# Kernel tuning notes

Hardware: AMD Instinct MI355X
Metric: run time of the kernel (lower is better)

The kernel has to match this reference:

```python
import jax, jax.numpy as jnp
import numpy as np

BLOCK, HALO, HEADS = 8, 4, 4


def setup_inputs() -> dict:
    key = jax.random.key(0)
    ks = jax.random.split(key, 9)
    B, C, H, W = 8, 256, 64, 64
    inner = C  # heads * dim_head = 4 * 64
    d = inner // HEADS
    R = BLOCK + 2 * HALO  # 16
    s = 0.02
    return {
        "x": jax.random.normal(ks[0], (B, C, H, W), jnp.float32),
        "wq": jax.random.normal(ks[1], (inner, C), jnp.float32) * s,
        "wkv": jax.random.normal(ks[2], (2 * inner, C), jnp.float32) * s,
        "wo": jax.random.normal(ks[3], (C, inner), jnp.float32) * s,
        "bo": jax.random.normal(ks[4], (C,), jnp.float32) * s,
        "rel_h": jax.random.normal(ks[5], (2 * R - 1, d), jnp.float32) * (d ** -0.5),
        "rel_w": jax.random.normal(ks[6], (2 * R - 1, d), jnp.float32) * (d ** -0.5),
        "w_conv": jax.random.normal(ks[7], (4 * C, C), jnp.float32) * s,
        "b_conv": jax.random.normal(ks[8], (4 * C,), jnp.float32) * s,
    }


def reference(x, wq, wkv, wo, bo, rel_h, rel_w, w_conv, b_conv):
    B, C, H, W = x.shape
    bs, halo, heads = BLOCK, HALO, HEADS
    R = bs + 2 * halo
    inner = wq.shape[0]
    d = inner // heads
    nh, nw = H // bs, W // bs
    Nb = B * nh * nw

    # ---- HaloAttention ----
    # block queries: (B, C, nh, bs, nw, bs) -> (Nb, bs*bs, C)
    q_in = x.reshape(B, C, nh, bs, nw, bs).transpose(0, 2, 4, 3, 5, 1).reshape(Nb, bs * bs, C)
    # haloed K/V windows via overlapping gather (== F.unfold(kernel=R, stride=bs, pad=halo))
    xp = jnp.pad(x, ((0, 0), (0, 0), (halo, halo), (halo, halo)))
    ridx = (jnp.arange(nh) * bs)[:, None] + jnp.arange(R)[None]  # (nh, R)
    cidx = (jnp.arange(nw) * bs)[:, None] + jnp.arange(R)[None]  # (nw, R)
    win = xp[:, :, ridx][:, :, :, :, cidx]                       # (B, C, nh, R, nw, R)
    kv_in = win.transpose(0, 2, 4, 3, 5, 1).reshape(Nb, R * R, C)

    q = (q_in @ wq.T).reshape(Nb, bs * bs, heads, d).transpose(0, 2, 1, 3) * (d ** -0.5)
    kv = kv_in @ wkv.T
    k, v = jnp.split(kv, 2, axis=-1)
    k = k.reshape(Nb, R * R, heads, d).transpose(0, 2, 1, 3)
    v = v.reshape(Nb, R * R, heads, d).transpose(0, 2, 1, 3)

    sim = jnp.einsum('bhid,bhjd->bhij', q, k)  # (Nb, heads, bs*bs, R*R)

    # relative position logits (computed from the scaled q, as in the torch code)
    q5 = q.reshape(Nb, heads, bs, bs, d)
    rel_idx = jnp.arange(R)[None, :] - jnp.arange(bs)[:, None] + (R - 1)  # (bs, R)
    lw = jnp.einsum('bhxyd,yjd->bhxyj', q5, rel_w[rel_idx])  # over key col j
    lh = jnp.einsum('bhxyd,xid->bhxyi', q5, rel_h[rel_idx])  # over key row i
    sim = sim.reshape(Nb, heads, bs, bs, R, R) + lw[..., None, :] + lh[..., None]
    sim = sim.reshape(Nb, heads, bs * bs, R * R)

    # mask out padded halo positions
    m = jnp.pad(jnp.ones((H, W), bool), ((halo, halo), (halo, halo)))
    mwin = m[ridx][:, :, cidx].transpose(0, 2, 1, 3).reshape(nh * nw, R * R)
    mask = jnp.broadcast_to(mwin[None], (B, nh * nw, R * R)).reshape(Nb, 1, 1, R * R)
    sim = jnp.where(mask, sim, -jnp.finfo(sim.dtype).max)

    attn = jax.nn.softmax(sim, axis=-1)
    out = jnp.einsum('bhij,bhjd->bhid', attn, v)
    out = out.transpose(0, 2, 1, 3).reshape(Nb, bs * bs, inner)
    out = out @ wo.T + bo  # (Nb, bs*bs, C)
    y = out.reshape(B, nh, nw, bs, bs, C).transpose(0, 5, 1, 3, 2, 4).reshape(B, C, H, W)

    # ---- Conv2d(dim, 4*dim, 1) + PixelShuffle(2) ----
    y = jnp.einsum('bchw,oc->bohw', y, w_conv) + b_conv[None, :, None, None]
    Cn = y.shape[1] // 4
    y = y.reshape(B, Cn, 2, 2, H, W).transpose(0, 1, 4, 2, 5, 3).reshape(B, Cn, 2 * H, 2 * W)
    return y
```

## Files before the change

### kernel.cpp

```cpp
#include <hip/hip_runtime.h>

typedef unsigned short u16;
typedef unsigned int u32;
typedef __attribute__((ext_vector_type(8))) short short8;
typedef __attribute__((ext_vector_type(4))) float f32x4;

__device__ __forceinline__ float bf2f(u16 u){ union { u32 i; float f; } x; x.i = ((u32)u)<<16; return x.f; }
__device__ __forceinline__ u16 f2bf(float f){ union { float f; u32 i; } x; x.f = f; u32 r = x.i + 0x7fffu + ((x.i>>16)&1u); return (u16)(r>>16); }

#define MFMA16(a,b,c) __builtin_amdgcn_mfma_f32_16x16x32_bf16((a),(b),(c),0,0,0)

__device__ __forceinline__ uint4 ld8(const void* p, size_t off, int f32) {
  if (f32) {
    const float* fp = (const float*)p + off;
    float4 a = *(const float4*)fp;
    float4 b = *(const float4*)(fp + 4);
    uint4 o;
    o.x = (u32)f2bf(a.x) | ((u32)f2bf(a.y)<<16);
    o.y = (u32)f2bf(a.z) | ((u32)f2bf(a.w)<<16);
    o.z = (u32)f2bf(b.x) | ((u32)f2bf(b.y)<<16);
    o.w = (u32)f2bf(b.z) | ((u32)f2bf(b.w)<<16);
    return o;
  }
  return *(const uint4*)((const u16*)p + off);
}
__device__ __forceinline__ uint2 ld4(const void* p, size_t off, int f32) {
  if (f32) {
    const float* fp = (const float*)p + off;
    float4 a = *(const float4*)fp;
    uint2 o;
    o.x = (u32)f2bf(a.x) | ((u32)f2bf(a.y)<<16);
    o.y = (u32)f2bf(a.z) | ((u32)f2bf(a.w)<<16);
    return o;
  }
  return *(const uint2*)((const u16*)p + off);
}
__device__ __forceinline__ float ldsc(const void* p, size_t off, int f32) {
  if (f32) return ((const float*)p)[off];
  return bf2f(((const u16*)p)[off]);
}

__global__ __launch_bounds__(256) void k_detect(const u32* __restrict__ x, int* __restrict__ flag)
{
  __shared__ int cnt;
  if (threadIdx.x == 0) cnt = 0;
  __syncthreads();
  int c = 0;
  #pragma unroll
  for (int i = 0; i < 32; ++i) {
    u32 w = x[threadIdx.x*32 + i];
    u32 e = (w >> 7) & 0xFFu;
    c += (e == 0u || (e >= 96u && e <= 143u)) ? 1 : 0;
  }
  atomicAdd(&cnt, c);
  __syncthreads();
  if (threadIdx.x == 0) *flag = (cnt < 4915) ? 1 : 0;
}

__global__ __launch_bounds__(256) void k_transpose(const void* __restrict__ x, u16* __restrict__ xt,
                                                   const int* __restrict__ flagp)
{
  __shared__ int sflag;
  __shared__ __align__(16) u16 tile[64][68];
  if (threadIdx.x == 0) sflag = *flagp;
  __syncthreads();
  const int f32 = sflag;
  const int p0 = blockIdx.x*64, c0 = blockIdx.y*64, b = blockIdx.z;
  const int t = threadIdx.x;
  const size_t xbo = ((size_t)(b*256 + c0))*4096 + p0;
  #pragma unroll
  for (int pass=0; pass<4; ++pass) {
    int cl = pass*16 + (t>>4);
    int pl = (t&15)*4;
    uint2 v = ld4(x, xbo + (size_t)cl*4096 + pl, f32);
    *(uint2*)&tile[cl][pl] = v;
  }
  __syncthreads();
  u16* xtb = xt + ((size_t)b*4096 + p0)*256 + c0;
  #pragma unroll
  for (int pass=0; pass<4; ++pass) {
    int pl = pass*16 + (t>>4);
    int cl = (t&15)*4;
    unsigned int lo = (unsigned int)tile[cl][pl]   | ((unsigned int)tile[cl+1][pl]<<16);
    unsigned int hi = (unsigned int)tile[cl+2][pl] | ((unsigned int)tile[cl+3][pl]<<16);
    uint2 o; o.x = lo; o.y = hi;
    *(uint2*)(xtb + (size_t)pl*256 + cl) = o;
  }
}

__global__ __launch_bounds__(256) void k_gemm_bt(
  const u16* __restrict__ A, const void* __restrict__ Bt, const void* __restrict__ bias,
  void* __restrict__ C, int M, int N, int K, float scale, int shuffle,
  const int* __restrict__ flagp)
{
  __shared__ int sflag;
  __shared__ __align__(16) char smem[20608];
  u16* Als = (u16*)smem;
  u16* Bls = (u16*)(smem + 10240);
  if (threadIdx.x == 0) sflag = *flagp;
  __syncthreads();
  const int f32 = sflag;
  const int m0 = blockIdx.x*128, n0 = blockIdx.y*128;
  const int t = threadIdx.x, lane = t & 63, wv = t >> 6;
  const int wm = (wv & 1)*64, wn = (wv >> 1)*64;
  const int lm = lane & 15, lq = lane >> 4;
  f32x4 acc[4][4] = {};
  for (int k0 = 0; k0 < K; k0 += 32) {
    #pragma unroll
    for (int i = 0; i < 2; ++i) {
      int u = t + i*256;
      int row = u >> 2, ch = (u & 3)*8;
      *(uint4*)&Als[row*40 + ch] = *(const uint4*)(A + (size_t)(m0+row)*K + k0 + ch);
      *(uint4*)&Bls[row*40 + ch] = ld8(Bt, (size_t)(n0+row)*K + k0 + ch, f32);
    }
    __syncthreads();
    short8 af[4], bf[4];
    #pragma unroll
    for (int i=0;i<4;++i) af[i] = *(const short8*)&Als[(wm + i*16 + lm)*40 + lq*8];
    #pragma unroll
    for (int i=0;i<4;++i) bf[i] = *(const short8*)&Bls[(wn + i*16 + lm)*40 + lq*8];
    #pragma unroll
    for (int mt=0;mt<4;++mt)
      #pragma unroll
      for (int nt=0;nt<4;++nt)
        acc[mt][nt] = MFMA16(af[mt], bf[nt], acc[mt][nt]);
    __syncthreads();
  }

  if (!shuffle) {
    u16* eh = (u16*)smem;
    #pragma unroll
    for (int c=0;c<2;++c) {
      __syncthreads();
      if ((wv>>1) == c) {
        #pragma unroll
        for (int nt=0;nt<4;++nt) {
          int col = n0 + c*64 + nt*16 + lm;
          float bv = bias ? ldsc(bias, col, f32) : 0.0f;
          #pragma unroll
          for (int mt=0;mt<4;++mt)
            #pragma unroll
            for (int r=0;r<4;++r) {
              int row = wm + mt*16 + lq*4 + r;
              eh[row*72 + nt*16 + lm] = f2bf(acc[mt][nt][r]*scale + bv);
            }
        }
      }
      __syncthreads();
      {
        int row = t >> 1, off = (t & 1)*32;
        const uint4* s = (const uint4*)&eh[row*72 + off];
        uint4 v0 = s[0], v1 = s[1], v2 = s[2], v3 = s[3];
        uint4* dp = (uint4*)((u16*)C + (size_t)(m0+row)*N + n0 + c*64 + off);
        dp[0]=v0; dp[1]=v1; dp[2]=v2; dp[3]=v3;
      }
    }
  } else {
    float* ef = (float*)smem;
    const int b = m0 >> 12;
    const int hh0 = (m0 & 4095) >> 6;
    #pragma unroll
    for (int c=0;c<4;++c) {
      __syncthreads();
      if ((wv>>1) == (c>>1)) {
        #pragma unroll
        for (int nt2=0;nt2<2;++nt2) {
          int nt = (c&1)*2 + nt2;
          int col = n0 + wn + nt*16 + lm;
          float bv = bias ? ldsc(bias, col, f32) : 0.0f;
          int col_rel = nt2*16 + lm;
          int cn_rel = col_rel >> 2, rr = (col_rel >> 1) & 1, ss = col_rel & 1;
          #pragma unroll
          for (int mt=0;mt<4;++mt)
            #pragma unroll
            for (int r=0;r<4;++r) {
              int row = wm + mt*16 + lq*4 + r;
              int orow = cn_rel*4 + (row>>6)*2 + rr;
              int ow   = (row & 63)*2 + ss;
              ef[orow*136 + ow] = acc[mt][nt][r]*scale + bv;
            }
        }
      }
      __syncthreads();
      {
        int orow = t >> 3, seg = t & 7;
        int cn_rel = orow >> 2, oh_rel = orow & 3;
        int cn = ((n0 + c*32) >> 2) + cn_rel;
        size_t obase = (((size_t)(b*256 + cn))*128 + hh0*2 + oh_rel)*128 + seg*16;
        const float4* s = (const float4*)&ef[orow*136 + seg*16];
        float4 v0 = s[0], v1 = s[1], v2 = s[2], v3 = s[3];
        if (f32) {
          float4* dp = (float4*)((float*)C + obase);
          dp[0]=v0; dp[1]=v1; dp[2]=v2; dp[3]=v3;
        } else {
          float vv[16];
          *(float4*)&vv[0]=v0; *(float4*)&vv[4]=v1; *(float4*)&vv[8]=v2; *(float4*)&vv[12]=v3;
          u32 pw[8];
          #pragma unroll
          for (int j=0;j<8;++j) pw[j] = (u32)f2bf(vv[2*j]) | ((u32)f2bf(vv[2*j+1])<<16);
          u16* dp = (u16*)C + obase;
          *(uint4*)dp       = *(uint4*)&pw[0];
          *(uint4*)(dp + 8) = *(uint4*)&pw[4];
        }
      }
    }
  }
}

#define MASKVAL (-30000.0f)
__global__ __launch_bounds__(256) void k_halo_attn(
  const u16* __restrict__ qo, const u16* __restrict__ kv,
  const void* __restrict__ relh, const void* __restrict__ relw,
  u16* __restrict__ aout, const int* __restrict__ flagp)
{
  __shared__ int sflag;
  __shared__ __align__(16) u16 Qs[64*72];
  __shared__ __align__(16) u16 KP[128*72];
  __shared__ __align__(16) u16 Vt[64*136];
  __shared__ __align__(16) u16 Gw[64*32];
  __shared__ __align__(16) u16 Gh[64*32];
  if (threadIdx.x == 0) sflag = *flagp;
  __syncthreads();
  const int f32 = sflag;

  const int blk = blockIdx.x, head = blockIdx.y;
  const int bb = blk >> 6, by = (blk >> 3) & 7, bx = blk & 7;
  const int h0 = by*8, w0 = bx*8;
  const int t = threadIdx.x, lane = t & 63, wv = t >> 6;
  const int lm = lane & 15, lq = lane >> 4;
  const size_t pixbase = (size_t)bb * 4096;
  const float LOG2E = 1.4426950408889634f;

  #pragma unroll
  for (int i=0;i<2;++i) {
    int u = t + i*256;
    int row = u >> 3, ch = (u & 7)*8;
    int qx = row >> 3, qy = row & 7;
    size_t p = pixbase + (size_t)(h0+qx)*64 + (w0+qy);
    *(uint4*)&Qs[row*72 + ch] = *(const uint4*)(qo + p*256 + head*64 + ch);
  }
  {
    u16* RW = KP; u16* RH = KP + 2048;
    if (t < 248) {
      *(uint4*)&RW[t*8] = ld8(relw, (size_t)t*8, f32);
      *(uint4*)&RH[t*8] = ld8(relh, (size_t)t*8, f32);
    } else {
      uint4 z; z.x=z.y=z.z=z.w=0;
      int o = 1984 + (t-248)*8;
      *(uint4*)&RW[o] = z;
      *(uint4*)&RH[o] = z;
    }
  }
  __syncthreads();
  {
    const u16* RW = KP; const u16* RH = KP + 2048;
    f32x4 agw[2] = {}, agh[2] = {};
    #pragma unroll
    for (int ks=0;ks<2;++ks) {
      short8 aq = *(const short8*)&Qs[(wv*16 + lm)*72 + ks*32 + lq*8];
      #pragma unroll
      for (int nt=0;nt<2;++nt) {
        short8 bw = *(const short8*)&RW[(nt*16 + lm)*64 + ks*32 + lq*8];
        short8 bh = *(const short8*)&RH[(nt*16 + lm)*64 + ks*32 + lq*8];
        agw[nt] = MFMA16(aq, bw, agw[nt]);
        agh[nt] = MFMA16(aq, bh, agh[nt]);
      }
    }
    #pragma unroll
    for (int nt=0;nt<2;++nt)
      #pragma unroll
      for (int r=0;r<4;++r) {
        int m = wv*16 + lq*4 + r, c = nt*16 + lm;
        Gw[m*32 + c] = f2bf(agw[nt][r]);
        Gh[m*32 + c] = f2bf(agh[nt][r]);
      }
  }
  __syncthreads();

  float m_run[4], l_run[4];
  #pragma unroll
  for (int r=0;r<4;++r){ m_run[r] = MASKVAL; l_run[r] = 0.0f; }
  f32x4 acc_o[4] = {};

  for (int tile=0; tile<2; ++tile) {
    #pragma unroll
    for (int i=0;i<4;++i) {
      int u = t + i*256;
      int kl = u >> 3, ch = (u & 7)*8;
      int ki = tile*8 + (kl >> 4), kj = kl & 15;
      int hk = h0 - 4 + ki, wk = w0 - 4 + kj;
      uint4 v; v.x=v.y=v.z=v.w=0;
      if ((unsigned)hk < 64u && (unsigned)wk < 64u) {
        size_t p = pixbase + (size_t)hk*64 + wk;
        v = *(const uint4*)(kv + p*512 + head*64 + ch);
      }
      *(uint4*)&KP[kl*72 + ch] = v;
    }
    {
      int kl = t & 127, db = (t >> 7)*32;
      int ki = tile*8 + (kl >> 4), kj = kl & 15;
      int hk = h0 - 4 + ki, wk = w0 - 4 + kj;
      bool ok = ((unsigned)hk < 64u) && ((unsigned)wk < 64u);
      size_t p = pixbase + (size_t)hk*64 + wk;
      const u16* vp = kv + p*512 + 256 + head*64 + db;
      #pragma unroll
      for (int c=0;c<4;++c) {
        union { uint4 v; u16 s[8]; } uu;
        uu.v.x=uu.v.y=uu.v.z=uu.v.w=0;
        if (ok) uu.v = *(const uint4*)(vp + c*8);
        #pragma unroll
        for (int jj=0;jj<8;++jj) Vt[(db + c*8 + jj)*136 + kl] = uu.s[jj];
      }
    }
    __syncthreads();
    f32x4 as[8] = {};
    #pragma unroll
    for (int ks=0;ks<2;++ks) {
      short8 aq = *(const short8*)&Qs[(wv*16 + lm)*72 + ks*32 + lq*8];
      #pragma unroll
      for (int nt=0;nt<8;++nt) {
        short8 bk = *(const short8*)&KP[(nt*16 + lm)*72 + ks*32 + lq*8];
        as[nt] = MFMA16(aq, bk, as[nt]);
      }
    }
    __syncthreads();
    #pragma unroll
    for (int r=0;r<4;++r) {
      int m = wv*16 + lq*4 + r;
      int qx = m >> 3, qy = m & 7;
      float vals[8]; float rowmax = MASKVAL;
      #pragma unroll
      for (int nt=0;nt<8;++nt) {
        int ki = tile*8 + nt;
        int hk = h0 - 4 + ki, wk = w0 - 4 + lm;
        float v = as[nt][r]
                + bf2f(Gw[m*32 + (lm - qy + 15)])
                + bf2f(Gh[m*32 + (ki - qx + 15)]);
        if (!((unsigned)hk < 64u && (unsigned)wk < 64u)) v = MASKVAL;
        vals[nt] = v;
        rowmax = fmaxf(rowmax, v);
      }
      #pragma unroll
      for (int s=1;s<16;s<<=1) rowmax = fmaxf(rowmax, __shfl_xor(rowmax, s, 64));
      float mnew = fmaxf(m_run[r], rowmax);
      float alpha = exp2f((m_run[r] - mnew)*LOG2E);
      float rs = 0.0f;
      #pragma unroll
      for (int nt=0;nt<8;++nt) {
        float e = exp2f((vals[nt] - mnew)*LOG2E);
        rs += e;
        KP[m*136 + nt*16 + lm] = f2bf(e);
      }
      #pragma unroll
      for (int s=1;s<16;s<<=1) rs += __shfl_xor(rs, s, 64);
      l_run[r] = l_run[r]*alpha + rs;
      m_run[r] = mnew;
      #pragma unroll
      for (int nt=0;nt<4;++nt) acc_o[nt][r] *= alpha;
    }
    __syncthreads();
    #pragma unroll
    for (int ks=0;ks<4;++ks) {
      short8 ap = *(const short8*)&KP[(wv*16 + lm)*136 + ks*32 + lq*8];
      #pragma unroll
      for (int nt=0;nt<4;++nt) {
        short8 bv = *(const short8*)&Vt[(nt*16 + lm)*136 + ks*32 + lq*8];
        acc_o[nt] = MFMA16(ap, bv, acc_o[nt]);
      }
    }
    __syncthreads();
  }
  #pragma unroll
  for (int nt=0;nt<4;++nt)
    #pragma unroll
    for (int r=0;r<4;++r) {
      int m = wv*16 + lq*4 + r;
      int qx = m >> 3, qy = m & 7;
      size_t p = pixbase + (size_t)(h0+qx)*64 + (w0+qy);
      aout[p*256 + head*64 + nt*16 + lm] = f2bf(acc_o[nt][r]/l_run[r]);
    }
}

extern "C" void kernel_launch(void* const* d_in, const int* in_sizes, int n_in,
                              void* d_out, int out_size, void* d_ws, size_t ws_size,
                              hipStream_t stream)
{
  const void* x     = d_in[0];
  const void* wq    = d_in[1];
  const void* wkv   = d_in[2];
  const void* wo    = d_in[3];
  const void* bo    = d_in[4];
  const void* relh  = d_in[5];
  const void* relw  = d_in[6];
  const void* wconv = d_in[7];
  const void* bconv = d_in[8];

  int* flag = (int*)d_ws;
  u16* y2   = (u16*)((char*)d_ws + 4096);
  u16* base = (u16*)d_out;
  u16* kvb  = base;
  u16* qo   = base + 16777216;
  u16* xt   = base + 25165824;
  u16* aout = qo;

  k_detect<<<1, 256, 0, stream>>>((const u32*)x, flag);
  k_transpose<<<dim3(64,4,8), 256, 0, stream>>>(x, xt, flag);
  k_gemm_bt<<<dim3(256,2), 256, 0, stream>>>(xt, wq,  nullptr, qo,  32768, 256, 256, 0.125f, 0, flag);
  k_gemm_bt<<<dim3(256,4), 256, 0, stream>>>(xt, wkv, nullptr, kvb, 32768, 512, 256, 1.0f,   0, flag);
  k_halo_attn<<<dim3(512,4), 256, 0, stream>>>(qo, kvb, relh, relw, aout, flag);
  k_gemm_bt<<<dim3(256,2), 256, 0, stream>>>(aout, wo, bo, y2, 32768, 256, 256, 1.0f, 0, flag);
  k_gemm_bt<<<dim3(256,8), 256, 0, stream>>>(y2, wconv, bconv, d_out, 32768, 1024, 256, 1.0f, 1, flag);
}
```

Baseline: 408.7 us.

## Fuse Q/KV projections into one GEMM and double-buffer GEMM LDS tiles

```diff
diff --git a/kernel.cpp b/kernel.cpp
--- a/kernel.cpp
+++ b/kernel.cpp
@@ -89,31 +89,52 @@
 }
 
 __global__ __launch_bounds__(256) void k_gemm_bt(
-  const u16* __restrict__ A, const void* __restrict__ Bt, const void* __restrict__ bias,
-  void* __restrict__ C, int M, int N, int K, float scale, int shuffle,
+  const u16* __restrict__ A, int lda,
+  const void* __restrict__ Bt0, const void* __restrict__ Bt1, int nsplit,
+  const void* __restrict__ bias,
+  void* __restrict__ C, int M, int N, int K,
+  float s_lo, float s_hi, int shuffle,
   const int* __restrict__ flagp)
 {
   __shared__ int sflag;
-  __shared__ __align__(16) char smem[20608];
-  u16* Als = (u16*)smem;
-  u16* Bls = (u16*)(smem + 10240);
+  __shared__ __align__(16) char smem[40960];
   if (threadIdx.x == 0) sflag = *flagp;
   __syncthreads();
   const int f32 = sflag;
   const int m0 = blockIdx.x*128, n0 = blockIdx.y*128;
+  const void* Bs; int boff;
+  if (Bt1 && n0 >= nsplit) { Bs = Bt1; boff = n0 - nsplit; } else { Bs = Bt0; boff = n0; }
   const int t = threadIdx.x, lane = t & 63, wv = t >> 6;
   const int wm = (wv & 1)*64, wn = (wv >> 1)*64;
   const int lm = lane & 15, lq = lane >> 4;
   f32x4 acc[4][4] = {};
+  uint4 pa[2], pb[2];
+  #pragma unroll
+  for (int i=0;i<2;++i) {
+    int u = t + i*256, row = u >> 2, ch = (u & 3)*8;
+    pa[i] = *(const uint4*)(A + (size_t)(m0+row)*lda + ch);
+    pb[i] = ld8(Bs, (size_t)(boff+row)*K + ch, f32);
+  }
+  int cur = 0;
   for (int k0 = 0; k0 < K; k0 += 32) {
-    #pragma unroll
-    for (int i = 0; i < 2; ++i) {
-      int u = t + i*256;
-      int row = u >> 2, ch = (u & 3)*8;
-      *(uint4*)&Als[row*40 + ch] = *(const uint4*)(A + (size_t)(m0+row)*K + k0 + ch);
-      *(uint4*)&Bls[row*40 + ch] = ld8(Bt, (size_t)(n0+row)*K + k0 + ch, f32);
+    u16* Als = (u16*)(smem + cur*20480);
+    u16* Bls = (u16*)(smem + cur*20480 + 10240);
+    #pragma unroll
+    for (int i=0;i<2;++i) {
+      int u = t + i*256, row = u >> 2, ch = (u & 3)*8;
+      *(uint4*)&Als[row*40 + ch] = pa[i];
+      *(uint4*)&Bls[row*40 + ch] = pb[i];
     }
     __syncthreads();
+    if (k0 + 32 < K) {
+      int k1 = k0 + 32;
+      #pragma unroll
+      for (int i=0;i<2;++i) {
+        int u = t + i*256, row = u >> 2, ch = (u & 3)*8;
+        pa[i] = *(const uint4*)(A + (size_t)(m0+row)*lda + k1 + ch);
+        pb[i] = ld8(Bs, (size_t)(boff+row)*K + k1 + ch, f32);
+      }
+    }
     short8 af[4], bf[4];
     #pragma unroll
     for (int i=0;i<4;++i) af[i] = *(const short8*)&Als[(wm + i*16 + lm)*40 + lq*8];
@@ -124,7 +145,7 @@
       #pragma unroll
       for (int nt=0;nt<4;++nt)
         acc[mt][nt] = MFMA16(af[mt], bf[nt], acc[mt][nt]);
-    __syncthreads();
+    cur ^= 1;
   }
 
   if (!shuffle) {
@@ -136,13 +157,14 @@
         #pragma unroll
         for (int nt=0;nt<4;++nt) {
           int col = n0 + c*64 + nt*16 + lm;
+          float sc = (col < nsplit) ? s_lo : s_hi;
           float bv = bias ? ldsc(bias, col, f32) : 0.0f;
           #pragma unroll
           for (int mt=0;mt<4;++mt)
             #pragma unroll
             for (int r=0;r<4;++r) {
               int row = wm + mt*16 + lq*4 + r;
-              eh[row*72 + nt*16 + lm] = f2bf(acc[mt][nt][r]*scale + bv);
+              eh[row*72 + nt*16 + lm] = f2bf(acc[mt][nt][r]*sc + bv);
             }
         }
       }
@@ -177,7 +199,7 @@
               int row = wm + mt*16 + lq*4 + r;
               int orow = cn_rel*4 + (row>>6)*2 + rr;
               int ow   = (row & 63)*2 + ss;
-              ef[orow*136 + ow] = acc[mt][nt][r]*scale + bv;
+              ef[orow*136 + ow] = acc[mt][nt][r]*s_hi + bv;
             }
         }
       }
@@ -209,9 +231,9 @@
 
 #define MASKVAL (-30000.0f)
 __global__ __launch_bounds__(256) void k_halo_attn(
-  const u16* __restrict__ qo, const u16* __restrict__ kv,
+  u16* __restrict__ qkv,
   const void* __restrict__ relh, const void* __restrict__ relw,
-  u16* __restrict__ aout, const int* __restrict__ flagp)
+  const int* __restrict__ flagp)
 {
   __shared__ int sflag;
   __shared__ __align__(16) u16 Qs[64*72];
@@ -237,7 +259,7 @@
     int row = u >> 3, ch = (u & 7)*8;
     int qx = row >> 3, qy = row & 7;
     size_t p = pixbase + (size_t)(h0+qx)*64 + (w0+qy);
-    *(uint4*)&Qs[row*72 + ch] = *(const uint4*)(qo + p*256 + head*64 + ch);
+    *(uint4*)&Qs[row*72 + ch] = *(const uint4*)(qkv + p*768 + head*64 + ch);
   }
   {
     u16* RW = KP; u16* RH = KP + 2048;
@@ -292,7 +314,7 @@
       uint4 v; v.x=v.y=v.z=v.w=0;
       if ((unsigned)hk < 64u && (unsigned)wk < 64u) {
         size_t p = pixbase + (size_t)hk*64 + wk;
-        v = *(const uint4*)(kv + p*512 + head*64 + ch);
+        v = *(const uint4*)(qkv + p*768 + 256 + head*64 + ch);
       }
       *(uint4*)&KP[kl*72 + ch] = v;
     }
@@ -302,7 +324,7 @@
       int hk = h0 - 4 + ki, wk = w0 - 4 + kj;
       bool ok = ((unsigned)hk < 64u) && ((unsigned)wk < 64u);
       size_t p = pixbase + (size_t)hk*64 + wk;
-      const u16* vp = kv + p*512 + 256 + head*64 + db;
+      const u16* vp = qkv + p*768 + 512 + head*64 + db;
       #pragma unroll
       for (int c=0;c<4;++c) {
         union { uint4 v; u16 s[8]; } uu;
@@ -377,7 +399,7 @@
       int m = wv*16 + lq*4 + r;
       int qx = m >> 3, qy = m & 7;
       size_t p = pixbase + (size_t)(h0+qx)*64 + (w0+qy);
-      aout[p*256 + head*64 + nt*16 + lm] = f2bf(acc_o[nt][r]/l_run[r]);
+      qkv[p*768 + head*64 + nt*16 + lm] = f2bf(acc_o[nt][r]/l_run[r]);
     }
 }
 
@@ -398,16 +420,16 @@
   int* flag = (int*)d_ws;
   u16* y2   = (u16*)((char*)d_ws + 4096);
   u16* base = (u16*)d_out;
-  u16* kvb  = base;
-  u16* qo   = base + 16777216;
+  u16* qkv  = base;
   u16* xt   = base + 25165824;
-  u16* aout = qo;
 
   k_detect<<<1, 256, 0, stream>>>((const u32*)x, flag);
   k_transpose<<<dim3(64,4,8), 256, 0, stream>>>(x, xt, flag);
-  k_gemm_bt<<<dim3(256,2), 256, 0, stream>>>(xt, wq,  nullptr, qo,  32768, 256, 256, 0.125f, 0, flag);
-  k_gemm_bt<<<dim3(256,4), 256, 0, stream>>>(xt, wkv, nullptr, kvb, 32768, 512, 256, 1.0f,   0, flag);
-  k_halo_attn<<<dim3(512,4), 256, 0, stream>>>(qo, kvb, relh, relw, aout, flag);
-  k_gemm_bt<<<dim3(256,2), 256, 0, stream>>>(aout, wo, bo, y2, 32768, 256, 256, 1.0f, 0, flag);
-  k_gemm_bt<<<dim3(256,8), 256, 0, stream>>>(y2, wconv, bconv, d_out, 32768, 1024, 256, 1.0f, 1, flag);
-}
+  k_gemm_bt<<<dim3(256,6), 256, 0, stream>>>(xt, 256, wq, wkv, 256, nullptr,
+                                             qkv, 32768, 768, 256, 0.125f, 1.0f, 0, flag);
+  k_halo_attn<<<dim3(512,4), 256, 0, stream>>>(qkv, relh, relw, flag);
+  k_gemm_bt<<<dim3(256,2), 256, 0, stream>>>(qkv, 768, wo, nullptr, 0, bo,
+                                             y2, 32768, 256, 256, 1.0f, 1.0f, 0, flag);
+  k_gemm_bt<<<dim3(256,8), 256, 0, stream>>>(y2, 256, wconv, nullptr, 0, bconv,
+                                             d_out, 32768, 1024, 256, 1.0f, 1.0f, 1, flag);
+}
```

Result: no change. 403.7 us (-1.2%).
